# Performance work log

Measured on AMD Instinct MI355X. Metric: run time of the kernel, lower is better.

Reference implementation:

```python
import jax, jax.numpy as jnp
import numpy as np

EPS = 1e-8  # torch F.cosine_similarity clamps norms at eps=1e-8


def setup_inputs() -> dict:
    key = jax.random.key(0)
    N, M, D = 1024, 20, 768  # speakers, utterances/speaker, embed dim
    embeddings = jax.random.normal(key, (N, M, D), dtype=jnp.float32)
    w = jnp.asarray(10.0, dtype=jnp.float32)  # init_w
    b = jnp.asarray(-5.0, dtype=jnp.float32)  # init_b
    return {"embeddings": embeddings, "w": w, "b": b}


def reference(embeddings, w, b):
    N, M, D = embeddings.shape
    centroids = embeddings.mean(axis=1)  # [N, D]
    # cosine similarity as one fused GEMM on normalized vectors
    e = embeddings / jnp.maximum(
        jnp.linalg.norm(embeddings, axis=-1, keepdims=True), EPS)
    c = centroids / jnp.maximum(
        jnp.linalg.norm(centroids, axis=-1, keepdims=True), EPS)
    # sim[j, i, m] = cos(e[i, m], centroid[j])  -- matches the torch loop/stack
    sim = jnp.einsum('imd,jd->jim', e, c)
    logits = w * sim + b  # [N_j, N_i, M]
    # torch: view(N*N, M).transpose(0,1).reshape(-1, N)
    #   => row index r = m*N + j, column i
    logits = jnp.transpose(logits, (2, 0, 1)).reshape(N * M, N)
    # torch labels: arange(N) expanded over M -> labels[r] = r // M
    labels = jnp.repeat(jnp.arange(N), M)
    logp = jax.nn.log_softmax(logits, axis=-1)
    loss = -jnp.mean(logp[jnp.arange(N * M), labels])
    return loss
```

## Files before the change

### kernel.cpp

```cpp
#include <hip/hip_runtime.h>
#include <hip/hip_bf16.h>
#include <cstdint>

#define N_SPK 1024
#define M_UTT 20
#define D_DIM 768
#define NM_ROWS (N_SPK * M_UTT)

static constexpr float EPS = 1e-8f;

#define WAIT_VM0   0x0F70
#define WAIT_VM8   0x0F78
#define WAIT_LGKM0 0xC07F

typedef __attribute__((ext_vector_type(4))) float floatx4;
typedef __attribute__((ext_vector_type(4))) int   intx4;
typedef __attribute__((ext_vector_type(8))) int   intx8;

__device__ __forceinline__ void load16_to_lds(const void* g, void* l) {
    __builtin_amdgcn_global_load_lds(
        (const __attribute__((address_space(1))) uint32_t*)g,
        (__attribute__((address_space(3))) uint32_t*)l, 16, 0, 0);
}

__device__ __forceinline__ float wave_sum(float v) {
    #pragma unroll
    for (int o = 32; o > 0; o >>= 1) v += __shfl_xor(v, o);
    return v;
}

__device__ __forceinline__ unsigned short fp8pk(float a, float b) {
    return (unsigned short)(__builtin_amdgcn_cvt_pk_fp8_f32(a, b, 0, false) & 0xFFFF);
}

__device__ __forceinline__ int kperm(int d) {
    return (d & ~63) | (((d >> 3) & 3) << 4) | (((d >> 5) & 1) << 3) | (d & 7);
}

__global__ __launch_bounds__(384) void prep_kernel(const float* __restrict__ emb,
                                                   unsigned char* __restrict__ ehat,
                                                   unsigned char* __restrict__ chat,
                                                   int* __restrict__ ctr,
                                                   float* __restrict__ accum) {
    const int i = blockIdx.x;
    const int t = threadIdx.x;
    const int wave = t >> 6, lane = t & 63;

    if (i == 0 && t == 0) { *ctr = 0; *accum = 0.f; }

    const float2* src = (const float2*)(emb + (size_t)i * M_UTT * D_DIM);
    const int dp = kperm(t * 2);

    float2 v[M_UTT];
    float ss[M_UTT];
    float2 cen = {0.f, 0.f};
    #pragma unroll
    for (int m = 0; m < M_UTT; ++m) {
        const float2 x = src[m * 384 + t];
        v[m] = x;
        ss[m] = x.x * x.x + x.y * x.y;
        cen.x += x.x; cen.y += x.y;
    }
    cen.x *= (1.f / M_UTT); cen.y *= (1.f / M_UTT);
    float css = cen.x * cen.x + cen.y * cen.y;

    __shared__ float red[M_UTT + 1][6];
    #pragma unroll
    for (int m = 0; m < M_UTT; ++m) {
        const float s = wave_sum(ss[m]);
        if (lane == 0) red[m][wave] = s;
    }
    {
        const float s = wave_sum(css);
        if (lane == 0) red[M_UTT][wave] = s;
    }
    __syncthreads();

    #pragma unroll
    for (int m = 0; m < M_UTT; ++m) {
        const float tot = red[m][0] + red[m][1] + red[m][2] +
                          red[m][3] + red[m][4] + red[m][5];
        const float rn = 1.0f / fmaxf(sqrtf(tot), EPS);
        *(unsigned short*)(ehat + ((size_t)(m * N_SPK + i)) * D_DIM + dp) =
            fp8pk(v[m].x * rn, v[m].y * rn);
    }
    {
        const float tot = red[M_UTT][0] + red[M_UTT][1] + red[M_UTT][2] +
                          red[M_UTT][3] + red[M_UTT][4] + red[M_UTT][5];
        const float rn = 1.0f / fmaxf(sqrtf(tot), EPS);
        *(unsigned short*)(chat + (size_t)i * D_DIM + dp) =
            fp8pk(cen.x * rn, cen.y * rn);
    }
}

__global__ __launch_bounds__(256, 2) void gemm_fused_kernel(
        const unsigned char* __restrict__ ehat,
        const unsigned char* __restrict__ chat,
        const float* __restrict__ wp,
        float* __restrict__ Psum,
        float* __restrict__ T) {
    __shared__ unsigned char As[2][128 * 128];
    __shared__ unsigned char Bs[2][128 * 128];

    const int t    = threadIdx.x;
    const int lane = t & 63;
    const int wid  = t >> 6;
    const int c    = lane & 15;
    const int quad = lane >> 4;
    const int wr   = wid >> 1;
    const int wc   = wid & 1;

    const int xcd = blockIdx.x & 7;
    const int idx = blockIdx.x >> 3;
    const int bu  = xcd * 20 + (idx >> 3);
    const int bj  = idx & 7;
    const int m   = bu >> 3;
    const int rb8 = bu & 7;
    const int u0  = bu * 128;
    const int j0  = bj * 128;

    const unsigned char* Ag = ehat + (size_t)u0 * D_DIM;
    const unsigned char* Bg = chat + (size_t)j0 * D_DIM;

    int goff[4];
    #pragma unroll
    for (int s = 0; s < 4; ++s) {
        const int ci  = s * 256 + t;
        const int row = ci >> 3;
        const int l   = (ci & 7) ^ (row & 7);
        goff[s] = row * D_DIM + l * 16;
    }

    int slotA[4], slotB[4];
    #pragma unroll
    for (int f = 0; f < 4; ++f) {
        const int rA = wr * 64 + f * 16 + c;
        const int rB = wc * 64 + f * 16 + c;
        slotA[f] = rA * 128 + ((quad ^ (c & 7)) * 16);
        slotB[f] = rB * 128 + ((quad ^ (c & 7)) * 16);
    }

    floatx4 acc[4][4] = {};

    #pragma unroll
    for (int s = 0; s < 4; ++s) {
        load16_to_lds(Ag + goff[s],       &As[0][(s * 256 + t) * 16]);
        load16_to_lds(Bg + goff[s],       &Bs[0][(s * 256 + t) * 16]);
    }
    #pragma unroll
    for (int s = 0; s < 4; ++s) {
        load16_to_lds(Ag + goff[s] + 128, &As[1][(s * 256 + t) * 16]);
        load16_to_lds(Bg + goff[s] + 128, &Bs[1][(s * 256 + t) * 16]);
    }
    __builtin_amdgcn_sched_barrier(0);

    #pragma unroll
    for (int kt = 0; kt < 6; ++kt) {
        const int cur = kt & 1;

        if (kt <= 4) __builtin_amdgcn_s_waitcnt(WAIT_VM8);
        else         __builtin_amdgcn_s_waitcnt(WAIT_VM0);
        __builtin_amdgcn_sched_barrier(0);
        __builtin_amdgcn_s_barrier();
        __builtin_amdgcn_sched_barrier(0);

        intx8 av[4], bv[4];
        #pragma unroll
        for (int f = 0; f < 4; ++f) {
            const intx4 lo = *(const intx4*)(&As[cur][slotA[f]]);
            const intx4 hi = *(const intx4*)(&As[cur][slotA[f] ^ 64]);
            av[f] = __builtin_shufflevector(lo, hi, 0, 1, 2, 3, 4, 5, 6, 7);
        }
        #pragma unroll
        for (int f = 0; f < 4; ++f) {
            const intx4 lo = *(const intx4*)(&Bs[cur][slotB[f]]);
            const intx4 hi = *(const intx4*)(&Bs[cur][slotB[f] ^ 64]);
            bv[f] = __builtin_shufflevector(lo, hi, 0, 1, 2, 3, 4, 5, 6, 7);
        }

        __builtin_amdgcn_s_setprio(1);
        #pragma unroll
        for (int it = 0; it < 4; ++it)
            #pragma unroll
            for (int jt = 0; jt < 4; ++jt)
                acc[it][jt] = __builtin_amdgcn_mfma_scale_f32_16x16x128_f8f6f4(
                    av[it], bv[jt], acc[it][jt],
                    0, 0,
                    0, 0x7F7F7F7F,
                    0, 0x7F7F7F7F);
        __builtin_amdgcn_s_setprio(0);

        if (kt < 4) {
            __builtin_amdgcn_s_waitcnt(WAIT_LGKM0);
            __builtin_amdgcn_sched_barrier(0);
            __builtin_amdgcn_s_barrier();
            __builtin_amdgcn_sched_barrier(0);
            const int k0 = (kt + 2) * 128;
            #pragma unroll
            for (int s = 0; s < 4; ++s) {
                load16_to_lds(Ag + goff[s] + k0, &As[cur][(s * 256 + t) * 16]);
                load16_to_lds(Bg + goff[s] + k0, &Bs[cur][(s * 256 + t) * 16]);
            }
            __builtin_amdgcn_sched_barrier(0);
        }
    }

    const float w = wp[0];
    const int rb320 = bu * 2 + wr;

    #pragma unroll
    for (int jt = 0; jt < 4; ++jt) {
        float sm = 0.f;
        #pragma unroll
        for (int it = 0; it < 4; ++it)
            #pragma unroll
            for (int r = 0; r < 4; ++r)
                sm += __expf(w * (acc[it][jt][r] - 1.0f));
        sm += __shfl_xor(sm, 16);
        sm += __shfl_xor(sm, 32);
        if (quad == 0)
            Psum[(size_t)rb320 * N_SPK + j0 + wc * 64 + jt * 16 + c] = sm;
    }

    #pragma unroll
    for (int it = 0; it < 4; ++it) {
        #pragma unroll
        for (int jt = 0; jt < 4; ++jt) {
            const int col = j0 + wc * 64 + jt * 16 + c;
            const int g = m * N_SPK + col;
            const int istar = g / M_UTT;
            const int rloc = rb8 * 128 + wr * 64 + it * 16 + quad * 4;
            #pragma unroll
            for (int r = 0; r < 4; ++r) {
                if (rloc + r == istar) T[g] = acc[it][jt][r];
            }
        }
    }
}

__global__ void combine_kernel(const float* __restrict__ Psum,
                               const float* __restrict__ T,
                               const float* __restrict__ wp,
                               int* __restrict__ ctr,
                               float* __restrict__ accum,
                               float* __restrict__ out) {
    const int p = blockIdx.x * 256 + threadIdx.x;
    const int m = p >> 10;
    const int j = p & 1023;
    const float w = wp[0];

    float S = 0.f;
    #pragma unroll
    for (int rb = 0; rb < 16; ++rb)
        S += Psum[(size_t)(m * 16 + rb) * N_SPK + j];
    const float term = w * (T[p] - 1.0f) - __logf(S);

    __shared__ float red[256];
    red[threadIdx.x] = term;
    __syncthreads();
    for (int o = 128; o > 0; o >>= 1) {
        if (threadIdx.x < o) red[threadIdx.x] += red[threadIdx.x + o];
        __syncthreads();
    }
    if (threadIdx.x == 0) {
        atomicAdd(accum, red[0]);
        __threadfence();
        const int old = atomicAdd(ctr, 1);
        if (old == 79) {
            const float a = atomicAdd(accum, 0.0f);
            out[0] = -a / (float)NM_ROWS;
        }
    }
}

extern "C" void kernel_launch(void* const* d_in, const int* in_sizes, int n_in,
                              void* d_out, int out_size, void* d_ws, size_t ws_size,
                              hipStream_t stream) {
    const float* emb = (const float*)d_in[0];
    const float* wp  = (const float*)d_in[1];
    float* out = (float*)d_out;

    char* ws = (char*)d_ws;
    unsigned char* ehat = (unsigned char*)(ws);
    unsigned char* chat = (unsigned char*)(ws + 15728640);
    float* Psum  = (float*)(ws + 16515072);
    float* T     = (float*)(ws + 17825792);
    int*   ctr   = (int*)  (ws + 17907712);
    float* accum = (float*)(ws + 17907716);

    prep_kernel<<<dim3(N_SPK), dim3(384), 0, stream>>>(emb, ehat, chat, ctr, accum);
    gemm_fused_kernel<<<dim3(1280), dim3(256), 0, stream>>>(ehat, chat, wp, Psum, T);
    combine_kernel<<<dim3(80), dim3(256), 0, stream>>>(Psum, T, wp, ctr, accum, out);
}
```

Baseline: 129.9 us.

## Load B tile via registers with swizzled LDS stores instead of direct global-to-LDS

B tiles now come in through global loads into registers and are written to LDS with swizzled stores, with a one-stage register prefetch ahead of the LDS double buffer. The A tiles still use direct global-to-LDS loads. The aim is to read B rows contiguously from global memory rather than in a permuted order, and to overlap B fetches with compute. The cost is more VGPRs, extra LDS write instructions and added lgkm waits. The VM wait counts are unchanged even though fewer LDS-direct loads are now in flight, which may make the waits looser or tighter than intended.

```diff
diff --git a/kernel.cpp b/kernel.cpp
--- a/kernel.cpp
+++ b/kernel.cpp
@@ -104,9 +104,9 @@
 
     const int t    = threadIdx.x;
     const int lane = t & 63;
-    const int wid  = t >> 6;
     const int c    = lane & 15;
     const int quad = lane >> 4;
+    const int wid  = t >> 6;
     const int wr   = wid >> 1;
     const int wc   = wid & 1;
 
@@ -123,12 +123,14 @@
     const unsigned char* Bg = chat + (size_t)j0 * D_DIM;
 
     int goff[4];
+    int boffB[4], bdst[4];
     #pragma unroll
     for (int s = 0; s < 4; ++s) {
         const int ci  = s * 256 + t;
         const int row = ci >> 3;
-        const int l   = (ci & 7) ^ (row & 7);
-        goff[s] = row * D_DIM + l * 16;
+        goff[s]  = row * D_DIM + (((ci & 7) ^ (row & 7)) * 16);
+        boffB[s] = row * D_DIM + ((ci & 7) * 16);
+        bdst[s]  = row * 128 + (((ci & 7) ^ (row & 7)) * 16);
     }
 
     int slotA[4], slotB[4];
@@ -141,28 +143,42 @@
     }
 
     floatx4 acc[4][4] = {};
-
-    #pragma unroll
-    for (int s = 0; s < 4; ++s) {
-        load16_to_lds(Ag + goff[s],       &As[0][(s * 256 + t) * 16]);
-        load16_to_lds(Bg + goff[s],       &Bs[0][(s * 256 + t) * 16]);
-    }
-    #pragma unroll
-    for (int s = 0; s < 4; ++s) {
+    intx4 breg[4];
+
+    #pragma unroll
+    for (int s = 0; s < 4; ++s)
+        load16_to_lds(Ag + goff[s], &As[0][(s * 256 + t) * 16]);
+    intx4 b0[4], b1[4];
+    #pragma unroll
+    for (int s = 0; s < 4; ++s) b0[s] = *(const intx4*)(Bg + boffB[s]);
+    #pragma unroll
+    for (int s = 0; s < 4; ++s) b1[s] = *(const intx4*)(Bg + boffB[s] + 128);
+    #pragma unroll
+    for (int s = 0; s < 4; ++s)
         load16_to_lds(Ag + goff[s] + 128, &As[1][(s * 256 + t) * 16]);
-        load16_to_lds(Bg + goff[s] + 128, &Bs[1][(s * 256 + t) * 16]);
-    }
+    #pragma unroll
+    for (int s = 0; s < 4; ++s) *(intx4*)(&Bs[0][bdst[s]]) = b0[s];
+    #pragma unroll
+    for (int s = 0; s < 4; ++s) *(intx4*)(&Bs[1][bdst[s]]) = b1[s];
+    #pragma unroll
+    for (int s = 0; s < 4; ++s) breg[s] = *(const intx4*)(Bg + boffB[s] + 256);
+    __builtin_amdgcn_s_waitcnt(WAIT_LGKM0);
+    __builtin_amdgcn_sched_barrier(0);
+    __builtin_amdgcn_s_barrier();
     __builtin_amdgcn_sched_barrier(0);
 
     #pragma unroll
     for (int kt = 0; kt < 6; ++kt) {
         const int cur = kt & 1;
 
-        if (kt <= 4) __builtin_amdgcn_s_waitcnt(WAIT_VM8);
-        else         __builtin_amdgcn_s_waitcnt(WAIT_VM0);
-        __builtin_amdgcn_sched_barrier(0);
-        __builtin_amdgcn_s_barrier();
-        __builtin_amdgcn_sched_barrier(0);
+        if (kt > 0) {
+            if (kt < 5) __builtin_amdgcn_s_waitcnt(WAIT_VM8);
+            else        __builtin_amdgcn_s_waitcnt(WAIT_VM0);
+            __builtin_amdgcn_s_waitcnt(WAIT_LGKM0);
+            __builtin_amdgcn_sched_barrier(0);
+            __builtin_amdgcn_s_barrier();
+            __builtin_amdgcn_sched_barrier(0);
+        }
 
         intx8 av[4], bv[4];
         #pragma unroll
@@ -197,9 +213,15 @@
             __builtin_amdgcn_sched_barrier(0);
             const int k0 = (kt + 2) * 128;
             #pragma unroll
-            for (int s = 0; s < 4; ++s) {
+            for (int s = 0; s < 4; ++s)
                 load16_to_lds(Ag + goff[s] + k0, &As[cur][(s * 256 + t) * 16]);
-                load16_to_lds(Bg + goff[s] + k0, &Bs[cur][(s * 256 + t) * 16]);
+            #pragma unroll
+            for (int s = 0; s < 4; ++s) *(intx4*)(&Bs[cur][bdst[s]]) = breg[s];
+            if (kt < 3) {
+                const int k1 = (kt + 3) * 128;
+                #pragma unroll
+                for (int s = 0; s < 4; ++s)
+                    breg[s] = *(const intx4*)(Bg + boffB[s] + k1);
             }
             __builtin_amdgcn_sched_barrier(0);
         }
```

Result: no change. 130.3 us (+0.3%).
